# Optimization experiments

Measured on AMD Instinct MI355X. Metric: run time of the kernel, lower is better.

The kernel has to match this reference:

```python
import jax, jax.numpy as jnp
import numpy as np

SCALE = 1.0 / (64 ** 0.5)  # 1/sqrt(dim_key)

def setup_inputs() -> dict:
    key = jax.random.key(0)
    ks = jax.random.split(key, 8)
    B, S, D, H, dk = 4, 2048, 1024, 16, 64
    s = 0.02
    return {
        "values": jax.random.normal(ks[0], (B, S, D), jnp.float32),
        "queries": jax.random.normal(ks[1], (B, S, D), jnp.float32),
        "keys": jax.random.normal(ks[2], (B, S, D), jnp.float32),
        "Wq": jax.random.normal(ks[3], (H, D, dk), jnp.float32) * s,
        "bq": jnp.zeros((H, dk), jnp.float32),
        "Wk": jax.random.normal(ks[4], (H, D, dk), jnp.float32) * s,
        "bk": jnp.zeros((H, dk), jnp.float32),
        "Wv": jax.random.normal(ks[5], (H, D, dk), jnp.float32) * s,
        "bv": jnp.zeros((H, dk), jnp.float32),
        "Wo": jax.random.normal(ks[6], (D, D), jnp.float32) * s,
        "bo": jnp.zeros((D,), jnp.float32),
    }

def reference(values, queries, keys, Wq, bq, Wk, bk, Wv, bv, Wo, bo):
    # Per-head projections, batched across heads: [B,S,D] x [H,D,dk] -> [B,H,S,dk]
    q = jnp.einsum('bsd,hdk->bhsk', queries, Wq) + bq[None, :, None, :]
    k = jnp.einsum('bsd,hdk->bhsk', keys, Wk) + bk[None, :, None, :]
    v = jnp.einsum('bsd,hdk->bhsk', values, Wv) + bv[None, :, None, :]
    # Scaled dot-product scores [B,H,S,S]
    scores = jnp.einsum('bhqk,bhsk->bhqs', q, k) * SCALE
    S = scores.shape[-1]
    causal = jnp.tril(jnp.ones((S, S), bool))
    scores = jnp.where(causal, scores, jnp.float32(-1e19))
    attn = jax.nn.softmax(scores, axis=-1)
    ctx = jnp.einsum('bhqs,bhsk->bhqk', attn, v)  # [B,H,S,dk]
    # Concat heads along last axis (head-major, matching tf.concat order)
    B, H, Sq, dk = ctx.shape
    ctx = jnp.transpose(ctx, (0, 2, 1, 3)).reshape(B, Sq, H * dk)
    return ctx @ Wo + bo
```

## Files before the change

### kernel.cpp

```cpp
#include <hip/hip_runtime.h>
#include <hip/hip_bf16.h>
#include <cstdint>

#define B_ 4
#define H_ 16
#define S_ 2048
#define D_ 1024
#define DK 64
#define QSCALE 0.18033688f

typedef float f32x4 __attribute__((ext_vector_type(4)));
typedef short bf8 __attribute__((ext_vector_type(8)));
typedef unsigned short u16;

__device__ __forceinline__ u16 f2bf(float x){
  union { float f; uint32_t u; } c; c.f = x;
  uint32_t u = c.u;
  uint32_t r = (u + 0x7FFFu + ((u >> 16) & 1u)) >> 16;
  return (u16)r;
}

__device__ __forceinline__ uint32_t pk2bf(float a, float b){
  __hip_bfloat162 t = __float22bfloat162_rn(make_float2(a, b));
  uint32_t r; __builtin_memcpy(&r, &t, 4); return r;
}

__device__ __forceinline__ void gl16(const void* g, void* l){
  __builtin_amdgcn_global_load_lds(
      (const __attribute__((address_space(1))) void*)g,
      (__attribute__((address_space(3))) void*)l, 16, 0, 0);
}

__global__ __launch_bounds__(256) void cvt_in(
    const float* __restrict__ q, const float* __restrict__ k,
    const float* __restrict__ v, u16* __restrict__ o)
{
  const size_t N8 = (size_t)1 << 20;
  const size_t tot = 3 * N8;
  const size_t step = (size_t)gridDim.x * 256;
  for (size_t g0 = (size_t)blockIdx.x*256 + threadIdx.x; g0 < tot; g0 += step){
    int t = (int)(g0 >> 20);
    size_t r = g0 & (N8 - 1);
    const float* src = (t==0 ? q : (t==1 ? k : v));
    const float4* s4 = reinterpret_cast<const float4*>(src + r*8);
    float4 a = s4[0], b = s4[1];
    uint4 w;
    w.x = pk2bf(a.x,a.y); w.y = pk2bf(a.z,a.w);
    w.z = pk2bf(b.x,b.y); w.w = pk2bf(b.z,b.w);
    *reinterpret_cast<uint4*>(o + ((size_t)t << 23) + r*8) = w;
  }
}

__global__ __launch_bounds__(256) void wtrans3(
    const float* __restrict__ Wq, const float* __restrict__ Wk,
    const float* __restrict__ Wv, u16* __restrict__ oq,
    u16* __restrict__ ok, u16* __restrict__ ov)
{
  __shared__ u16 T[64*72];
  const int tid = threadIdx.x;
  const int z = blockIdx.z, t = z >> 4, hh = z & 15;
  const float* src = (t==0 ? Wq : t==1 ? Wk : Wv) + (size_t)hh * (D_*DK);
  u16* dst = (t==0 ? oq : t==1 ? ok : ov) + (size_t)hh * (DK*D_);
  const int r0 = blockIdx.y*64;
  #pragma unroll
  for (int p=0;p<4;++p){
    int r  = p*16 + (tid>>4);
    int c4 = (tid&15)*4;
    float4 v = *reinterpret_cast<const float4*>(&src[(size_t)(r0+r)*DK + c4]);
    uint2 w; w.x = pk2bf(v.x, v.y); w.y = pk2bf(v.z, v.w);
    *reinterpret_cast<uint2*>(&T[r*72 + c4]) = w;
  }
  __syncthreads();
  const int c = tid>>2, rg = (tid&3)*16;
  u16 tmp[16];
  #pragma unroll
  for (int i=0;i<16;++i) tmp[i] = T[(rg+i)*72 + c];
  *reinterpret_cast<bf8*>(&dst[(size_t)c*D_ + r0 + rg])     = *reinterpret_cast<bf8*>(&tmp[0]);
  *reinterpret_cast<bf8*>(&dst[(size_t)c*D_ + r0 + rg + 8]) = *reinterpret_cast<bf8*>(&tmp[8]);
}

__global__ __launch_bounds__(256) void wtrans(
    const float* __restrict__ in, u16* __restrict__ out, int R, int C)
{
  __shared__ u16 T[64*72];
  const int tid = threadIdx.x;
  const int r0 = blockIdx.y*64, c0 = blockIdx.x*64;
  #pragma unroll
  for (int p=0;p<4;++p){
    int r  = p*16 + (tid>>4);
    int c4 = (tid&15)*4;
    float4 v = *reinterpret_cast<const float4*>(&in[(size_t)(r0+r)*C + c0 + c4]);
    uint2 w; w.x = pk2bf(v.x, v.y); w.y = pk2bf(v.z, v.w);
    *reinterpret_cast<uint2*>(&T[r*72 + c4]) = w;
  }
  __syncthreads();
  const int c = tid>>2, rg = (tid&3)*16;
  u16 tmp[16];
  #pragma unroll
  for (int i=0;i<16;++i) tmp[i] = T[(rg+i)*72 + c];
  *reinterpret_cast<bf8*>(&out[(size_t)(c0+c)*R + r0 + rg])     = *reinterpret_cast<bf8*>(&tmp[0]);
  *reinterpret_cast<bf8*>(&out[(size_t)(c0+c)*R + r0 + rg + 8]) = *reinterpret_cast<bf8*>(&tmp[8]);
}

__global__ __launch_bounds__(256) void gemm_qkv(
    const u16* __restrict__ Ab,
    const u16* __restrict__ Bq, const u16* __restrict__ Bk,
    const u16* __restrict__ Bv,
    const float* __restrict__ bq, const float* __restrict__ bk,
    const float* __restrict__ bv,
    u16* __restrict__ oq, u16* __restrict__ ok, u16* __restrict__ ov)
{
  __shared__ u16 As[2][128*64];
  __shared__ u16 Bs[2][128*64];
  const int tid = threadIdx.x;
  const int wid = tid>>6, lane = tid&63, g = lane>>4, l15 = lane&15;
  const int z = blockIdx.x >> 9, bid = blockIdx.x & 511;
  const u16* A     = Ab + ((size_t)z << 23);
  const u16*   Bt  = (z==0 ? Bq : z==1 ? Bk : Bv);
  const float* bias= (z==0 ? bq : z==1 ? bk : bv);
  u16* Out         = (z==0 ? oq : z==1 ? ok : ov);
  const float osc  = (z==0 ? QSCALE : 1.0f);
  const int xcd = bid & 7, i = bid >> 3;
  const int cb = i & 7, rb = xcd*8 + (i>>3);
  const int row0 = rb*128, col0 = cb*128;
  const int wr = wid>>1, wc = wid&1;

  f32x4 acc[4][4];
  #pragma unroll
  for (int m=0;m<4;++m)
    #pragma unroll
    for (int n=0;n<4;++n) acc[m][n] = (f32x4){0.f,0.f,0.f,0.f};

  auto STAGE = [&](int buf, int k0){
    #pragma unroll
    for (int p=0;p<4;++p){
      int r0l = wid*32 + p*8;
      int row = r0l + (lane>>3);
      int ch = (lane&7) ^ (row&7);
      gl16(A  + (size_t)(row0+row)*D_ + k0 + ch*8, &As[buf][r0l*64]);
      gl16(Bt + (size_t)(col0+row)*D_ + k0 + ch*8, &Bs[buf][r0l*64]);
    }
  };

  int cur = 0;
  STAGE(0, 0);
  asm volatile("s_waitcnt vmcnt(0)" ::: "memory");
  __syncthreads();

  for (int k0 = 0; k0 < D_; k0 += 64) {
    if (k0 + 64 < D_) STAGE(cur^1, k0 + 64);

    bf8 af[4][2], bfm[4][2];
    #pragma unroll
    for (int m=0;m<4;++m){
      int row = wr*64 + m*16 + l15;
      af[m][0] = *reinterpret_cast<const bf8*>(&As[cur][row*64 + ((g     ^(row&7))*8)]);
      af[m][1] = *reinterpret_cast<const bf8*>(&As[cur][row*64 + (((4+g) ^(row&7))*8)]);
    }
    #pragma unroll
    for (int n=0;n<4;++n){
      int row = wc*64 + n*16 + l15;
      bfm[n][0] = *reinterpret_cast<const bf8*>(&Bs[cur][row*64 + ((g     ^(row&7))*8)]);
      bfm[n][1] = *reinterpret_cast<const bf8*>(&Bs[cur][row*64 + (((4+g) ^(row&7))*8)]);
    }
    #pragma unroll
    for (int m=0;m<4;++m)
      #pragma unroll
      for (int n=0;n<4;++n){
        acc[m][n] = __builtin_amdgcn_mfma_f32_16x16x32_bf16(af[m][0], bfm[n][0], acc[m][n], 0,0,0);
        acc[m][n] = __builtin_amdgcn_mfma_f32_16x16x32_bf16(af[m][1], bfm[n][1], acc[m][n], 0,0,0);
      }
    asm volatile("s_waitcnt vmcnt(0)" ::: "memory");
    __syncthreads();
    cur ^= 1;
  }

  #pragma unroll
  for (int m=0;m<4;++m){
    #pragma unroll
    for (int n=0;n<4;++n){
      int col = col0 + wc*64 + n*16 + l15;
      float bs = bias[col];
      if (z == 2){
        int rowb = row0 + wr*64 + m*16 + g*4;
        int b = rowb>>11, s = rowb&2047;
        int h = col>>6, dkk = col&63;
        ushort4 pk;
        pk.x = f2bf(acc[m][n][0]+bs); pk.y = f2bf(acc[m][n][1]+bs);
        pk.z = f2bf(acc[m][n][2]+bs); pk.w = f2bf(acc[m][n][3]+bs);
        *reinterpret_cast<ushort4*>(&Out[(((size_t)(b*H_+h)*DK)+dkk)*S_ + s]) = pk;
      } else {
        #pragma unroll
        for (int r=0;r<4;++r){
          int row = row0 + wr*64 + m*16 + g*4 + r;
          float v = (acc[m][n][r] + bs)*osc;
          int b = row>>11, s = row&2047;
          int h = col>>6, dkk = col&63;
          Out[(((size_t)(b*H_+h)*S_)+s)*DK + dkk] = f2bf(v);
        }
      }
    }
  }
}

__global__ __launch_bounds__(256) void gemm_out(
    const u16* __restrict__ A, const u16* __restrict__ Bt,
    const float* __restrict__ bias, float* __restrict__ Outp)
{
  __shared__ u16 As[2][128*64];
  __shared__ u16 Bs[2][128*64];
  const int tid = threadIdx.x;
  const int wid = tid>>6, lane = tid&63, g = lane>>4, l15 = lane&15;
  const int bid = blockIdx.x;
  const int xcd = bid & 7, i = bid >> 3;
  const int cb = i & 7, rb = xcd*8 + (i>>3);
  const int row0 = rb*128, col0 = cb*128;
  const int wr = wid>>1, wc = wid&1;

  f32x4 acc[4][4];
  #pragma unroll
  for (int m=0;m<4;++m)
    #pragma unroll
    for (int n=0;n<4;++n) acc[m][n] = (f32x4){0.f,0.f,0.f,0.f};

  auto STAGE = [&](int buf, int k0){
    #pragma unroll
    for (int p=0;p<4;++p){
      int r0l = wid*32 + p*8;
      int row = r0l + (lane>>3);
      int ch = (lane&7) ^ (row&7);
      gl16(A  + (size_t)(row0+row)*D_ + k0 + ch*8, &As[buf][r0l*64]);
      gl16(Bt + (size_t)(col0+row)*D_ + k0 + ch*8, &Bs[buf][r0l*64]);
    }
  };

  int cur = 0;
  STAGE(0, 0);
  asm volatile("s_waitcnt vmcnt(0)" ::: "memory");
  __syncthreads();

  for (int k0 = 0; k0 < D_; k0 += 64) {
    if (k0 + 64 < D_) STAGE(cur^1, k0 + 64);

    bf8 af[4][2], bfm[4][2];
    #pragma unroll
    for (int m=0;m<4;++m){
      int row = wr*64 + m*16 + l15;
      af[m][0] = *reinterpret_cast<const bf8*>(&As[cur][row*64 + ((g     ^(row&7))*8)]);
      af[m][1] = *reinterpret_cast<const bf8*>(&As[cur][row*64 + (((4+g) ^(row&7))*8)]);
    }
    #pragma unroll
    for (int n=0;n<4;++n){
      int row = wc*64 + n*16 + l15;
      bfm[n][0] = *reinterpret_cast<const bf8*>(&Bs[cur][row*64 + ((g     ^(row&7))*8)]);
      bfm[n][1] = *reinterpret_cast<const bf8*>(&Bs[cur][row*64 + (((4+g) ^(row&7))*8)]);
    }
    #pragma unroll
    for (int m=0;m<4;++m)
      #pragma unroll
      for (int n=0;n<4;++n){
        acc[m][n] = __builtin_amdgcn_mfma_f32_16x16x32_bf16(af[m][0], bfm[n][0], acc[m][n], 0,0,0);
        acc[m][n] = __builtin_amdgcn_mfma_f32_16x16x32_bf16(af[m][1], bfm[n][1], acc[m][n], 0,0,0);
      }
    asm volatile("s_waitcnt vmcnt(0)" ::: "memory");
    __syncthreads();
    cur ^= 1;
  }

  #pragma unroll
  for (int m=0;m<4;++m){
    #pragma unroll
    for (int n=0;n<4;++n){
      int col = col0 + wc*64 + n*16 + l15;
      float bs = bias[col];
      #pragma unroll
      for (int r=0;r<4;++r){
        int row = row0 + wr*64 + m*16 + g*4 + r;
        Outp[(size_t)row*D_ + col] = acc[m][n][r] + bs;
      }
    }
  }
}

__global__ __launch_bounds__(256) void attn_kernel(
    const u16* __restrict__ qp, const u16* __restrict__ kp,
    const u16* __restrict__ vt, u16* __restrict__ ctx)
{
  __shared__ u16 Kl[2][64*64];
  __shared__ u16 Vl[2][64*64];
  __shared__ u16 Pl[4][32*72];
  const int tid = threadIdx.x;
  const int wid = tid>>6, lane = tid&63, g = lane>>4, l15 = lane&15;
  const int bid0 = blockIdx.x;
  const int xx = bid0 & 7, yy = bid0 >> 3;
  const int bh = xx + 8*(yy >> 3);
  const int jj = yy & 7;
  const int b = bh >> 4, h = bh & 15;
  const size_t base = (size_t)bh * S_ * DK;

  bf8 ones;
  #pragma unroll
  for (int i=0;i<8;++i) ones[i] = (short)0x3F80;

  const int qts[2] = { jj, 15-jj };

  #pragma unroll 1
  for (int qi=0; qi<2; ++qi){
    const int qt = qts[qi];
    const int Q0 = qt*128;
    bf8 aq[2][2];
    #pragma unroll
    for (int qs=0;qs<2;++qs){
      int qrow = Q0 + wid*32 + qs*16 + l15;
      aq[qs][0] = *reinterpret_cast<const bf8*>(&qp[base + (size_t)qrow*DK +      g*8]);
      aq[qs][1] = *reinterpret_cast<const bf8*>(&qp[base + (size_t)qrow*DK + 32 + g*8]);
    }

    f32x4 acco[2][4], acc_l[2];
    #pragma unroll
    for (int qs=0;qs<2;++qs){
      #pragma unroll
      for (int nd=0;nd<4;++nd) acco[qs][nd] = (f32x4){0.f,0.f,0.f,0.f};
      acc_l[qs] = (f32x4){0.f,0.f,0.f,0.f};
    }

    auto STAGE = [&](int buf, int kt){
      const int k0 = kt*64;
      #pragma unroll
      for (int p=0;p<2;++p){
        int r0l = wid*16 + p*8;
        int row = r0l + (lane>>3);
        int ch  = (lane&7) ^ (row&7);
        gl16(kp + base + (size_t)(k0+row)*DK + ch*8, &Kl[buf][r0l*64]);
        gl16(vt + base + (size_t)row*S_ + k0 + ch*8, &Vl[buf][r0l*64]);
      }
    };

    const int nk = 2*qt + 2;
    int cur = 0;
    STAGE(cur, 0);
    asm volatile("s_waitcnt vmcnt(0)" ::: "memory");
    __syncthreads();

    for (int kt = 0; kt < nk; ++kt){
      if (kt < nk-1) STAGE(cur^1, kt+1);

      f32x4 sc[2][4];
      #pragma unroll
      for (int n=0;n<4;++n){
        int row = n*16 + l15;
        bf8 b0 = *reinterpret_cast<const bf8*>(&Kl[cur][row*64 + ((g     ^(row&7))*8)]);
        bf8 b1 = *reinterpret_cast<const bf8*>(&Kl[cur][row*64 + (((4+g) ^(row&7))*8)]);
        #pragma unroll
        for (int qs=0;qs<2;++qs){
          f32x4 z = (f32x4){0.f,0.f,0.f,0.f};
          z = __builtin_amdgcn_mfma_f32_16x16x32_bf16(aq[qs][0], b0, z, 0,0,0);
          z = __builtin_amdgcn_mfma_f32_16x16x32_bf16(aq[qs][1], b1, z, 0,0,0);
          sc[qs][n] = z;
        }
      }
      if (kt >= nk-2){
        const int k0 = kt*64;
        #pragma unroll
        for (int qs=0;qs<2;++qs){
          #pragma unroll
          for (int n=0;n<4;++n){
            #pragma unroll
            for (int r=0;r<4;++r){
              int qg = Q0 + wid*32 + qs*16 + g*4 + r;
              int kg = k0 + n*16 + l15;
              if (kg > qg) sc[qs][n][r] = -1e30f;
            }
          }
        }
      }
      #pragma unroll
      for (int qs=0;qs<2;++qs){
        #pragma unroll
        for (int n=0;n<4;++n){
          #pragma unroll
          for (int r=0;r<4;++r){
            float p = __builtin_amdgcn_exp2f(sc[qs][n][r]);
            union { float f; uint32_t u; } cu; cu.f = p;
            Pl[wid][(qs*16 + g*4 + r)*72 + n*16 + l15] = (u16)(cu.u >> 16);
          }
        }
      }
      asm volatile("s_waitcnt lgkmcnt(0)" ::: "memory");
      __builtin_amdgcn_sched_barrier(0);

      bf8 pa[2][2];
      #pragma unroll
      for (int qs=0;qs<2;++qs){
        pa[qs][0] = *reinterpret_cast<const bf8*>(&Pl[wid][(qs*16 + l15)*72 +      g*8]);
        pa[qs][1] = *reinterpret_cast<const bf8*>(&Pl[wid][(qs*16 + l15)*72 + 32 + g*8]);
        acc_l[qs] = __builtin_amdgcn_mfma_f32_16x16x32_bf16(pa[qs][0], ones, acc_l[qs], 0,0,0);
        acc_l[qs] = __builtin_amdgcn_mfma_f32_16x16x32_bf16(pa[qs][1], ones, acc_l[qs], 0,0,0);
      }
      #pragma unroll
      for (int nd=0;nd<4;++nd){
        int row = nd*16 + l15;
        bf8 v0 = *reinterpret_cast<const bf8*>(&Vl[cur][row*64 + ((g     ^(row&7))*8)]);
        bf8 v1 = *reinterpret_cast<const bf8*>(&Vl[cur][row*64 + (((4+g) ^(row&7))*8)]);
        #pragma unroll
        for (int qs=0;qs<2;++qs){
          acco[qs][nd] = __builtin_amdgcn_mfma_f32_16x16x32_bf16(pa[qs][0], v0, acco[qs][nd], 0,0,0);
          acco[qs][nd] = __builtin_amdgcn_mfma_f32_16x16x32_bf16(pa[qs][1], v1, acco[qs][nd], 0,0,0);
        }
      }
      asm volatile("s_waitcnt vmcnt(0)" ::: "memory");
      __syncthreads();
      cur ^= 1;
    }

    #pragma unroll
    for (int qs=0;qs<2;++qs){
      float rl[4];
      #pragma unroll
      for (int r=0;r<4;++r) rl[r] = __builtin_amdgcn_rcpf(acc_l[qs][r]);
      #pragma unroll
      for (int nd=0;nd<4;++nd){
        #pragma unroll
        for (int r=0;r<4;++r){
          int qg = Q0 + wid*32 + qs*16 + g*4 + r;
          float v = acco[qs][nd][r] * rl[r];
          ctx[((size_t)(b*S_) + qg)*D_ + h*DK + nd*16 + l15] = f2bf(v);
        }
      }
    }
  }
}

extern "C" void kernel_launch(void* const* d_in, const int* in_sizes, int n_in,
                              void* d_out, int out_size, void* d_ws, size_t ws_size,
                              hipStream_t stream)
{
  const float* values  = (const float*)d_in[0];
  const float* queries = (const float*)d_in[1];
  const float* keys    = (const float*)d_in[2];
  const float* Wq = (const float*)d_in[3];
  const float* bq = (const float*)d_in[4];
  const float* Wk = (const float*)d_in[5];
  const float* bk = (const float*)d_in[6];
  const float* Wv = (const float*)d_in[7];
  const float* bv = (const float*)d_in[8];
  const float* Wo = (const float*)d_in[9];
  const float* bo = (const float*)d_in[10];
  float* out = (float*)d_out;

  const size_t NE = (size_t)B_*H_*S_*DK;
  const size_t WE = (size_t)D_*D_;
  u16* cvt = (u16*)d_ws;
  u16* qp  = cvt + 3*NE;
  u16* kp  = qp + NE;
  u16* vtb = kp + NE;
  u16* wtq = vtb + NE;
  u16* wtk = wtq + WE;
  u16* wtv = wtk + WE;
  u16* wto = wtv + WE;
  u16* ctx = cvt;

  cvt_in<<<3072, 256, 0, stream>>>(queries, keys, values, cvt);
  wtrans3<<<dim3(1,16,48), 256, 0, stream>>>(Wq, Wk, Wv, wtq, wtk, wtv);
  wtrans<<<dim3(16,16,1), 256, 0, stream>>>(Wo, wto, D_, D_);
  gemm_qkv<<<1536, 256, 0, stream>>>(cvt, wtq, wtk, wtv,
                                     bq, bk, bv, qp, kp, vtb);
  attn_kernel<<<512, 256, 0, stream>>>(qp, kp, vtb, ctx);
  gemm_out<<<512, 256, 0, stream>>>(ctx, wto, bo, out);
}
```

Baseline: 186.5 us.

## Load K/V fragments directly from global memory and launch one query tile per block

Drops the LDS double-buffered K/V staging and its block-wide barriers. Each wave now reads K and V MFMA fragments straight from global memory into registers, with K prefetched one tile ahead in a ping-pong register pair. The grid doubles to one 128-row query tile per block, ordered longest-first in place of paired balanced tiles, and launch bounds ask for 3 blocks per SIMD. The aim is to remove sync overhead and raise occupancy, at the cost of every wave re-fetching K/V from L2 with less coalesced loads and higher register pressure.

```diff
diff --git a/kernel.cpp b/kernel.cpp
--- a/kernel.cpp
+++ b/kernel.cpp
@@ -282,150 +282,137 @@
   }
 }
 
-__global__ __launch_bounds__(256) void attn_kernel(
+__global__ __launch_bounds__(256, 3) void attn_kernel(
     const u16* __restrict__ qp, const u16* __restrict__ kp,
     const u16* __restrict__ vt, u16* __restrict__ ctx)
 {
-  __shared__ u16 Kl[2][64*64];
-  __shared__ u16 Vl[2][64*64];
   __shared__ u16 Pl[4][32*72];
   const int tid = threadIdx.x;
   const int wid = tid>>6, lane = tid&63, g = lane>>4, l15 = lane&15;
   const int bid0 = blockIdx.x;
   const int xx = bid0 & 7, yy = bid0 >> 3;
-  const int bh = xx + 8*(yy >> 3);
-  const int jj = yy & 7;
+  const int bh = xx + 8*(yy & 7);
+  const int qt = 15 - (yy >> 3);
   const int b = bh >> 4, h = bh & 15;
   const size_t base = (size_t)bh * S_ * DK;
+  const u16* kb = kp + base;
+  const u16* vb = vt + base;
 
   bf8 ones;
   #pragma unroll
   for (int i=0;i<8;++i) ones[i] = (short)0x3F80;
 
-  const int qts[2] = { jj, 15-jj };
-
-  #pragma unroll 1
-  for (int qi=0; qi<2; ++qi){
-    const int qt = qts[qi];
-    const int Q0 = qt*128;
-    bf8 aq[2][2];
-    #pragma unroll
-    for (int qs=0;qs<2;++qs){
-      int qrow = Q0 + wid*32 + qs*16 + l15;
-      aq[qs][0] = *reinterpret_cast<const bf8*>(&qp[base + (size_t)qrow*DK +      g*8]);
-      aq[qs][1] = *reinterpret_cast<const bf8*>(&qp[base + (size_t)qrow*DK + 32 + g*8]);
-    }
-
-    f32x4 acco[2][4], acc_l[2];
-    #pragma unroll
-    for (int qs=0;qs<2;++qs){
-      #pragma unroll
-      for (int nd=0;nd<4;++nd) acco[qs][nd] = (f32x4){0.f,0.f,0.f,0.f};
-      acc_l[qs] = (f32x4){0.f,0.f,0.f,0.f};
-    }
-
-    auto STAGE = [&](int buf, int kt){
-      const int k0 = kt*64;
-      #pragma unroll
-      for (int p=0;p<2;++p){
-        int r0l = wid*16 + p*8;
-        int row = r0l + (lane>>3);
-        int ch  = (lane&7) ^ (row&7);
-        gl16(kp + base + (size_t)(k0+row)*DK + ch*8, &Kl[buf][r0l*64]);
-        gl16(vt + base + (size_t)row*S_ + k0 + ch*8, &Vl[buf][r0l*64]);
-      }
-    };
-
-    const int nk = 2*qt + 2;
-    int cur = 0;
-    STAGE(cur, 0);
-    asm volatile("s_waitcnt vmcnt(0)" ::: "memory");
-    __syncthreads();
-
-    for (int kt = 0; kt < nk; ++kt){
-      if (kt < nk-1) STAGE(cur^1, kt+1);
-
-      f32x4 sc[2][4];
-      #pragma unroll
-      for (int n=0;n<4;++n){
-        int row = n*16 + l15;
-        bf8 b0 = *reinterpret_cast<const bf8*>(&Kl[cur][row*64 + ((g     ^(row&7))*8)]);
-        bf8 b1 = *reinterpret_cast<const bf8*>(&Kl[cur][row*64 + (((4+g) ^(row&7))*8)]);
+  const int Q0 = qt*128;
+  bf8 aq[2][2];
+  #pragma unroll
+  for (int qs=0;qs<2;++qs){
+    int qrow = Q0 + wid*32 + qs*16 + l15;
+    aq[qs][0] = *reinterpret_cast<const bf8*>(&qp[base + (size_t)qrow*DK +      g*8]);
+    aq[qs][1] = *reinterpret_cast<const bf8*>(&qp[base + (size_t)qrow*DK + 32 + g*8]);
+  }
+
+  f32x4 acco[2][4], acc_l[2];
+  #pragma unroll
+  for (int qs=0;qs<2;++qs){
+    #pragma unroll
+    for (int nd=0;nd<4;++nd) acco[qs][nd] = (f32x4){0.f,0.f,0.f,0.f};
+    acc_l[qs] = (f32x4){0.f,0.f,0.f,0.f};
+  }
+
+  const int nk = 2*qt + 2;
+
+  auto LK = [&](int kt, bf8 (&kf)[4][2]){
+    const u16* p = kb + (size_t)kt*64*DK;
+    #pragma unroll
+    for (int n=0;n<4;++n){
+      kf[n][0] = *reinterpret_cast<const bf8*>(&p[(n*16+l15)*DK +      g*8]);
+      kf[n][1] = *reinterpret_cast<const bf8*>(&p[(n*16+l15)*DK + 32 + g*8]);
+    }
+  };
+
+  bf8 kfA[4][2], kfB[4][2];
+  LK(0, kfA);
+
+  auto STEP = [&](int kt, bf8 (&kfc)[4][2], bf8 (&kfn)[4][2]){
+    const int k0 = kt*64;
+    bf8 vf[4][2];
+    #pragma unroll
+    for (int nd=0;nd<4;++nd){
+      vf[nd][0] = *reinterpret_cast<const bf8*>(&vb[(size_t)(nd*16+l15)*S_ + k0 +      g*8]);
+      vf[nd][1] = *reinterpret_cast<const bf8*>(&vb[(size_t)(nd*16+l15)*S_ + k0 + 32 + g*8]);
+    }
+    f32x4 sc[2][4];
+    #pragma unroll
+    for (int n=0;n<4;++n){
+      #pragma unroll
+      for (int qs=0;qs<2;++qs){
+        f32x4 z = (f32x4){0.f,0.f,0.f,0.f};
+        z = __builtin_amdgcn_mfma_f32_16x16x32_bf16(aq[qs][0], kfc[n][0], z, 0,0,0);
+        z = __builtin_amdgcn_mfma_f32_16x16x32_bf16(aq[qs][1], kfc[n][1], z, 0,0,0);
+        sc[qs][n] = z;
+      }
+    }
+    int ktn = (kt+1 < nk) ? kt+1 : kt;
+    LK(ktn, kfn);
+    if (kt >= nk-2){
+      #pragma unroll
+      for (int qs=0;qs<2;++qs)
         #pragma unroll
-        for (int qs=0;qs<2;++qs){
-          f32x4 z = (f32x4){0.f,0.f,0.f,0.f};
-          z = __builtin_amdgcn_mfma_f32_16x16x32_bf16(aq[qs][0], b0, z, 0,0,0);
-          z = __builtin_amdgcn_mfma_f32_16x16x32_bf16(aq[qs][1], b1, z, 0,0,0);
-          sc[qs][n] = z;
-        }
-      }
-      if (kt >= nk-2){
-        const int k0 = kt*64;
-        #pragma unroll
-        for (int qs=0;qs<2;++qs){
-          #pragma unroll
-          for (int n=0;n<4;++n){
-            #pragma unroll
-            for (int r=0;r<4;++r){
-              int qg = Q0 + wid*32 + qs*16 + g*4 + r;
-              int kg = k0 + n*16 + l15;
-              if (kg > qg) sc[qs][n][r] = -1e30f;
-            }
-          }
-        }
-      }
-      #pragma unroll
-      for (int qs=0;qs<2;++qs){
-        #pragma unroll
-        for (int n=0;n<4;++n){
+        for (int n=0;n<4;++n)
           #pragma unroll
           for (int r=0;r<4;++r){
-            float p = __builtin_amdgcn_exp2f(sc[qs][n][r]);
-            union { float f; uint32_t u; } cu; cu.f = p;
-            Pl[wid][(qs*16 + g*4 + r)*72 + n*16 + l15] = (u16)(cu.u >> 16);
+            int qg = Q0 + wid*32 + qs*16 + g*4 + r;
+            int kg = k0 + n*16 + l15;
+            if (kg > qg) sc[qs][n][r] = -1e30f;
           }
-        }
-      }
-      asm volatile("s_waitcnt lgkmcnt(0)" ::: "memory");
-      __builtin_amdgcn_sched_barrier(0);
-
-      bf8 pa[2][2];
-      #pragma unroll
-      for (int qs=0;qs<2;++qs){
-        pa[qs][0] = *reinterpret_cast<const bf8*>(&Pl[wid][(qs*16 + l15)*72 +      g*8]);
-        pa[qs][1] = *reinterpret_cast<const bf8*>(&Pl[wid][(qs*16 + l15)*72 + 32 + g*8]);
-        acc_l[qs] = __builtin_amdgcn_mfma_f32_16x16x32_bf16(pa[qs][0], ones, acc_l[qs], 0,0,0);
-        acc_l[qs] = __builtin_amdgcn_mfma_f32_16x16x32_bf16(pa[qs][1], ones, acc_l[qs], 0,0,0);
-      }
-      #pragma unroll
-      for (int nd=0;nd<4;++nd){
-        int row = nd*16 + l15;
-        bf8 v0 = *reinterpret_cast<const bf8*>(&Vl[cur][row*64 + ((g     ^(row&7))*8)]);
-        bf8 v1 = *reinterpret_cast<const bf8*>(&Vl[cur][row*64 + (((4+g) ^(row&7))*8)]);
-        #pragma unroll
-        for (int qs=0;qs<2;++qs){
-          acco[qs][nd] = __builtin_amdgcn_mfma_f32_16x16x32_bf16(pa[qs][0], v0, acco[qs][nd], 0,0,0);
-          acco[qs][nd] = __builtin_amdgcn_mfma_f32_16x16x32_bf16(pa[qs][1], v1, acco[qs][nd], 0,0,0);
-        }
-      }
-      asm volatile("s_waitcnt vmcnt(0)" ::: "memory");
-      __syncthreads();
-      cur ^= 1;
-    }
-
-    #pragma unroll
-    for (int qs=0;qs<2;++qs){
-      float rl[4];
-      #pragma unroll
-      for (int r=0;r<4;++r) rl[r] = __builtin_amdgcn_rcpf(acc_l[qs][r]);
-      #pragma unroll
-      for (int nd=0;nd<4;++nd){
+    }
+    #pragma unroll
+    for (int qs=0;qs<2;++qs)
+      #pragma unroll
+      for (int n=0;n<4;++n)
         #pragma unroll
         for (int r=0;r<4;++r){
-          int qg = Q0 + wid*32 + qs*16 + g*4 + r;
-          float v = acco[qs][nd][r] * rl[r];
-          ctx[((size_t)(b*S_) + qg)*D_ + h*DK + nd*16 + l15] = f2bf(v);
+          float p = __builtin_amdgcn_exp2f(sc[qs][n][r]);
+          union { float f; uint32_t u; } cu; cu.f = p;
+          Pl[wid][(qs*16 + g*4 + r)*72 + n*16 + l15] = (u16)(cu.u >> 16);
         }
+    asm volatile("s_waitcnt lgkmcnt(0)" ::: "memory");
+    __builtin_amdgcn_sched_barrier(0);
+
+    bf8 pa[2][2];
+    #pragma unroll
+    for (int qs=0;qs<2;++qs){
+      pa[qs][0] = *reinterpret_cast<const bf8*>(&Pl[wid][(qs*16 + l15)*72 +      g*8]);
+      pa[qs][1] = *reinterpret_cast<const bf8*>(&Pl[wid][(qs*16 + l15)*72 + 32 + g*8]);
+      acc_l[qs] = __builtin_amdgcn_mfma_f32_16x16x32_bf16(pa[qs][0], ones, acc_l[qs], 0,0,0);
+      acc_l[qs] = __builtin_amdgcn_mfma_f32_16x16x32_bf16(pa[qs][1], ones, acc_l[qs], 0,0,0);
+    }
+    #pragma unroll
+    for (int nd=0;nd<4;++nd)
+      #pragma unroll
+      for (int qs=0;qs<2;++qs){
+        acco[qs][nd] = __builtin_amdgcn_mfma_f32_16x16x32_bf16(pa[qs][0], vf[nd][0], acco[qs][nd], 0,0,0);
+        acco[qs][nd] = __builtin_amdgcn_mfma_f32_16x16x32_bf16(pa[qs][1], vf[nd][1], acco[qs][nd], 0,0,0);
+      }
+  };
+
+  for (int kt = 0; kt < nk; kt += 2){
+    STEP(kt,   kfA, kfB);
+    STEP(kt+1, kfB, kfA);
+  }
+
+  #pragma unroll
+  for (int qs=0;qs<2;++qs){
+    float rl[4];
+    #pragma unroll
+    for (int r=0;r<4;++r) rl[r] = __builtin_amdgcn_rcpf(acc_l[qs][r]);
+    #pragma unroll
+    for (int nd=0;nd<4;++nd){
+      #pragma unroll
+      for (int r=0;r<4;++r){
+        int qg = Q0 + wid*32 + qs*16 + g*4 + r;
+        float v = acco[qs][nd][r] * rl[r];
+        ctx[((size_t)(b*S_) + qg)*D_ + h*DK + nd*16 + l15] = f2bf(v);
       }
     }
   }
@@ -465,6 +452,6 @@
   wtrans<<<dim3(16,16,1), 256, 0, stream>>>(Wo, wto, D_, D_);
   gemm_qkv<<<1536, 256, 0, stream>>>(cvt, wtq, wtk, wtv,
                                      bq, bk, bv, qp, kp, vtb);
-  attn_kernel<<<512, 256, 0, stream>>>(qp, kp, vtb, ctx);
+  attn_kernel<<<1024, 256, 0, stream>>>(qp, kp, vtb, ctx);
   gemm_out<<<512, 256, 0, stream>>>(ctx, wto, bo, out);
 }
```

Result: slower. 288.1 us (+54.5%).
